# Optimization experiments

Hardware: AMD Instinct MI355X
Metric: run time of the kernel (lower is better)

The kernel has to match this reference:

```python
import jax, jax.numpy as jnp
import numpy as np

N_USERS = 100000
N_LOCAS = 50000
N = N_USERS + N_LOCAS
D = 128   # embedding_dynamic_size
K = 128   # kg entity dim
S = 128   # static dim
NK = 50000  # kg rows
E = 2048  # number of events
LN_EPS = 1e-5
NORM_EPS = 1e-12


def setup_inputs() -> dict:
    key = jax.random.key(0)
    ks = jax.random.split(key, 24)
    f = jnp.float32
    rin = D + K + 1
    s_rnn = 1.0 / np.sqrt(D)
    s_pred = 1.0 / np.sqrt(2 * S + 2 * D + K)
    inp = {
        'embedding': jax.random.normal(ks[0], (N, D), f),
        'static': jax.random.normal(ks[1], (N, S), f),
        'kg': jax.random.normal(ks[2], (NK, K), f),
        'W_ih_u': jax.random.normal(ks[3], (D, rin), f) * s_rnn,
        'b_ih_u': jax.random.normal(ks[4], (D,), f) * s_rnn,
        'W_hh_u': jax.random.normal(ks[5], (D, D), f) * s_rnn,
        'b_hh_u': jax.random.normal(ks[6], (D,), f) * s_rnn,
        'W_ih_l': jax.random.normal(ks[7], (D, rin), f) * s_rnn,
        'b_ih_l': jax.random.normal(ks[8], (D,), f) * s_rnn,
        'W_hh_l': jax.random.normal(ks[9], (D, D), f) * s_rnn,
        'b_hh_l': jax.random.normal(ks[10], (D,), f) * s_rnn,
        'w_proj': jax.random.normal(ks[11], (D,), f),   # NormalLinear(1, D) weight, std=1/sqrt(1)=1
        'b_proj': jax.random.normal(ks[12], (D,), f),
        'ln_g': jnp.ones((D + K,), f),
        'ln_b': jnp.zeros((D + K,), f),
        'W_pred': jax.random.normal(ks[13], (S + D, 2 * S + 2 * D + K), f) * s_pred,
        'b_pred': jnp.zeros((S + D,), f),
        'delta_u': jax.random.uniform(ks[14], (E,), f),
        'delta_l': jax.random.uniform(ks[15], (E,), f),
        'idx_user': jax.random.randint(ks[16], (E,), 0, N_USERS, jnp.int32),
        'idx_loca': jax.random.randint(ks[17], (E,), 0, N_LOCAS, jnp.int32),
        'idx_prev': jax.random.randint(ks[18], (E,), 0, N_LOCAS, jnp.int32),
        'idx_know': jax.random.randint(ks[19], (E,), 0, NK, jnp.int32),
        'num_users': N_USERS,
    }
    return inp


def reference(embedding, static, kg, W_ih_u, b_ih_u, W_hh_u, b_hh_u,
              W_ih_l, b_ih_l, W_hh_l, b_hh_l, w_proj, b_proj, ln_g, ln_b,
              W_pred, b_pred, delta_u, delta_l,
              idx_user, idx_loca, idx_prev, idx_know, num_users):
    sg = jax.lax.stop_gradient

    def l2n(x):  # F.normalize along the feature dim (row vector)
        return x / jnp.maximum(jnp.linalg.norm(x), NORM_EPS)

    # event index preprocessing (matches idx_loca + num_users etc.)
    xs = (idx_user, idx_loca + num_users, idx_prev + num_users, idx_know,
          delta_u, delta_l)

    def step(carry, ev):
        emb, loss = carry
        iu, il, ip, ik, du, dl = ev
        u = emb[iu]        # [D]
        l = emb[il]        # [D]
        p = emb[ip]        # [D]
        kgr = kg[ik]       # [K]
        # projection: u * (1 + Linear(1->D)(delta_u))
        proj = u * (1.0 + w_proj * du + b_proj)
        # layer_norm over concat([emb_prev, kg_row]) of size D+K
        x = jnp.concatenate([p, kgr])
        mu = x.mean()
        var = jnp.mean((x - mu) ** 2)
        ln = (x - mu) / jnp.sqrt(var + LN_EPS) * ln_g + ln_b
        meta = jnp.concatenate([proj, ln, static[ip], static[iu]])  # [2S+2D+K]
        pred = W_pred @ meta + b_pred                               # [S+D]
        tgt = jnp.concatenate([l, static[il]])
        loss_pred = jnp.mean((pred - sg(tgt)) ** 2)
        # RNNCell updates (tanh), then L2-normalize
        x_u = jnp.concatenate([l, kgr, du[None]])
        new_u = l2n(jnp.tanh(W_ih_u @ x_u + b_ih_u + W_hh_u @ u + b_hh_u))
        x_l = jnp.concatenate([u, kgr, dl[None]])
        new_l = l2n(jnp.tanh(W_ih_l @ x_l + b_ih_l + W_hh_l @ l + b_hh_l))
        loss = loss + loss_pred \
                    + jnp.mean((new_u - sg(u)) ** 2) \
                    + jnp.mean((new_l - sg(l)) ** 2)
        emb = emb.at[iu].set(new_u).at[il].set(new_l)
        return (emb, loss), None

    (emb, loss), _ = jax.lax.scan(
        step, (embedding, jnp.asarray(0.0, embedding.dtype)), xs)
    return emb, loss
```

## Files before the change

### kernel.cpp

```cpp
#include <hip/hip_runtime.h>

#define DEVINL static __device__ __forceinline__

typedef float f32x4 __attribute__((ext_vector_type(4)));

constexpr int NUSER = 100000;
constexpr int D     = 128;
constexpr int METAN = 640;
constexpr int NT    = 256;
constexpr int CH    = 4;
constexpr int KP4   = 160;
constexpr int KR4   = 96;
constexpr int NCPY  = 2048;
constexpr int STW   = 640;

struct Params {
  const float *emb_in, *stat, *kg;
  const float *Wihu, *bihu, *Whhu, *bhhu;
  const float *Wihl, *bihl, *Whhl, *bhhl;
  const float *wproj, *bproj, *lng, *lnb, *Wpred, *bpred;
  const float *deltau, *deltal;
  const int *idxu, *idxl, *idxp, *idxk;
  float *emb;
  float *loss_slot;
  float *WpredT;
  float *WrnnT;
  float *brnn;
  float *wcol;
  float *loss_ev;
  float *stash;
  int *cnt_u, *cnt_w, *cnt_t;
  int *flag_u, *flag_l;
  int E, N, NLOC, NWORK;
};

DEVINL float loadx(const float* p) {
  return __hip_atomic_load(p, __ATOMIC_RELAXED, __HIP_MEMORY_SCOPE_AGENT);
}
DEVINL void storex(float* p, float v) {
  __hip_atomic_store(p, v, __ATOMIC_RELAXED, __HIP_MEMORY_SCOPE_AGENT);
}
DEVINL int loadcnt(const int* p) {
  return __hip_atomic_load(p, __ATOMIC_RELAXED, __HIP_MEMORY_SCOPE_AGENT);
}
DEVINL void sigadd(int* pp) {
  __hip_atomic_fetch_add(pp, 1, __ATOMIC_RELAXED, __HIP_MEMORY_SCOPE_AGENT);
}
DEVINL float dot4(float4 a, float4 b) { return a.x*b.x + a.y*b.y + a.z*b.z + a.w*b.w; }

DEVINL float4 block_sum4(float4 v, float4* s4) {
  #pragma unroll
  for (int o = 32; o; o >>= 1) {
    v.x += __shfl_xor(v.x, o, 64); v.y += __shfl_xor(v.y, o, 64);
    v.z += __shfl_xor(v.z, o, 64); v.w += __shfl_xor(v.w, o, 64);
  }
  if ((threadIdx.x & 63) == 0) s4[threadIdx.x >> 6] = v;
  __syncthreads();
  float4 r;
  r.x = s4[0].x + s4[1].x + s4[2].x + s4[3].x;
  r.y = s4[0].y + s4[1].y + s4[2].y + s4[3].y;
  r.z = s4[0].z + s4[1].z + s4[2].z + s4[3].z;
  r.w = s4[0].w + s4[1].w + s4[2].w + s4[3].w;
  __syncthreads();
  return r;
}

DEVINL void half_sum4(float4 v, float4* s4, float4* lo, float4* hi) {
  #pragma unroll
  for (int o = 32; o; o >>= 1) {
    v.x += __shfl_xor(v.x, o, 64); v.y += __shfl_xor(v.y, o, 64);
    v.z += __shfl_xor(v.z, o, 64); v.w += __shfl_xor(v.w, o, 64);
  }
  if ((threadIdx.x & 63) == 0) s4[threadIdx.x >> 6] = v;
  __syncthreads();
  lo->x = s4[0].x + s4[1].x; lo->y = s4[0].y + s4[1].y;
  lo->z = s4[0].z + s4[1].z; lo->w = s4[0].w + s4[1].w;
  hi->x = s4[2].x + s4[3].x; hi->y = s4[2].y + s4[3].y;
  hi->z = s4[2].z + s4[3].z; hi->w = s4[2].w + s4[3].w;
  __syncthreads();
}

__global__ void k_init(Params p) {
  int tid = blockIdx.x * NT + threadIdx.x;
  int stride = gridDim.x * NT;
  for (int e = tid; e < p.E; e += stride) {
    p.flag_u[p.idxu[e]] = 1;
    p.flag_l[p.idxl[e]] = 1;
  }
  for (int idx = tid; idx < 256 * KP4; idx += stride) {
    int j = idx / KP4, k4 = idx - j * KP4;
    float4 v = *(const float4*)(p.Wpred + (size_t)j * METAN + k4 * 4);
    ((float4*)p.WpredT)[k4 * 256 + j] = v;
  }
  for (int idx = tid; idx < 256 * KR4; idx += stride) {
    int j = idx / KR4, k4 = idx - j * KR4;
    int i = j & 127;
    const float* Wih = (j < 128) ? p.Wihu : p.Wihl;
    const float* Whh = (j < 128) ? p.Whhu : p.Whhl;
    float4 v; float* vp = (float*)&v;
    #pragma unroll
    for (int e = 0; e < 4; ++e) {
      int k = k4 * 4 + e;
      vp[e] = (k < 256) ? Wih[(size_t)i * 257 + k] : Whh[(size_t)i * 128 + (k - 256)];
    }
    ((float4*)p.WrnnT)[k4 * 256 + j] = v;
  }
  for (int j = tid; j < 256; j += stride) {
    int i = j & 127;
    p.brnn[j] = (j < 128) ? p.bihu[i] + p.bhhu[i] : p.bihl[i] + p.bhhl[i];
    p.wcol[j] = (j < 128) ? p.Wihu[(size_t)i * 257 + 256] : p.Wihl[(size_t)i * 257 + 256];
  }
}

__global__ __launch_bounds__(NT) void k_copy(Params p) {
  size_t gid = (size_t)blockIdx.x * NT + threadIdx.x;
  size_t gs  = (size_t)gridDim.x * NT;
  size_t n4  = (size_t)p.N * 32;
  const f32x4* src = (const f32x4*)p.emb_in;
  f32x4* dst = (f32x4*)p.emb;
  size_t g = gid;
  for (; g + 3 * gs < n4; g += 4 * gs) {
    size_t g0 = g, g1 = g + gs, g2 = g + 2 * gs, g3 = g + 3 * gs;
    int r0 = (int)(g0 >> 5), r1 = (int)(g1 >> 5), r2 = (int)(g2 >> 5), r3 = (int)(g3 >> 5);
    int f0 = (r0 < NUSER) ? p.flag_u[r0] : p.flag_l[r0 - NUSER];
    int f1 = (r1 < NUSER) ? p.flag_u[r1] : p.flag_l[r1 - NUSER];
    int f2 = (r2 < NUSER) ? p.flag_u[r2] : p.flag_l[r2 - NUSER];
    int f3 = (r3 < NUSER) ? p.flag_u[r3] : p.flag_l[r3 - NUSER];
    f32x4 v0 = src[g0], v1 = src[g1], v2 = src[g2], v3 = src[g3];
    if (!f0) dst[g0] = v0;
    if (!f1) dst[g1] = v1;
    if (!f2) dst[g2] = v2;
    if (!f3) dst[g3] = v3;
  }
  for (; g < n4; g += gs) {
    int r = (int)(g >> 5);
    int f = (r < NUSER) ? p.flag_u[r] : p.flag_l[r - NUSER];
    f32x4 v = src[g];
    if (!f) dst[g] = v;
  }
}

__global__ __launch_bounds__(NT, 2) void k_chain(Params p) {
  __shared__ __align__(16) float s_u[CH][D], s_l[CH][D], s_p[CH][D], s_kg[CH][D];
  __shared__ float4 s_r4[4];
  __shared__ unsigned long long s_redu[4][CH];
  __shared__ int s_ev[8][CH];
  __shared__ float s_dd[2][CH];

  const int tid = threadIdx.x, w = tid >> 6, lane = tid & 63;
  const int c = blockIdx.x;
  const int base = c * CH;
  const int nev = min(CH, p.E - base);
  if (nev <= 0) return;

  int iu_[CH], il_[CH], ip_[CH], ik_[CH];
  float du_[CH], dl_[CH];
  #pragma unroll
  for (int e = 0; e < CH; ++e) {
    int t = base + e; bool v = e < nev;
    iu_[e] = v ? p.idxu[t] : -1;
    il_[e] = v ? p.idxl[t] : -1;
    ip_[e] = v ? p.idxp[t] : -1;
    ik_[e] = v ? p.idxk[t] : 0;
    du_[e] = v ? p.deltau[t] : 0.f;
    dl_[e] = v ? p.deltal[t] : 0.f;
  }

  unsigned long long pk[CH] = {0ull,0ull,0ull,0ull};
  for (int s = tid; s < base; s += NT) {
    int ius = p.idxu[s], ils = p.idxl[s], ips = p.idxp[s];
    #pragma unroll
    for (int e = 0; e < CH; ++e) {
      unsigned long long a  = (ius == iu_[e]);
      unsigned long long wl = (ils == il_[e]);
      unsigned long long b  = (unsigned long long)((ils == il_[e]) + (ips == il_[e]));
      unsigned long long cc = (ils == ip_[e]);
      pk[e] += a | (wl << 16) | (b << 32) | (cc << 48);
    }
  }
  #pragma unroll
  for (int o = 32; o; o >>= 1) {
    #pragma unroll
    for (int e = 0; e < CH; ++e) pk[e] += __shfl_xor(pk[e], o, 64);
  }
  if (lane == 0) {
    #pragma unroll
    for (int e = 0; e < CH; ++e) s_redu[w][e] = pk[e];
  }
  __syncthreads();
  #pragma unroll
  for (int e = 0; e < CH; ++e)
    pk[e] = s_redu[0][e] + s_redu[1][e] + s_redu[2][e] + s_redu[3][e];
  __syncthreads();

  int A_[CH], WL_[CH], B_[CH], C_[CH];
  #pragma unroll
  for (int e = 0; e < CH; ++e) {
    int a  = (int)(pk[e] & 0xffff),        wl = (int)((pk[e] >> 16) & 0xffff);
    int b  = (int)((pk[e] >> 32) & 0xffff), cc = (int)((pk[e] >> 48) & 0xffff);
    #pragma unroll
    for (int s2 = 0; s2 < CH; ++s2) if (s2 < e) {
      a  += (iu_[s2] == iu_[e]);
      wl += (il_[s2] == il_[e]);
      b  += (il_[s2] == il_[e]) + (ip_[s2] == il_[e]);
      cc += (il_[s2] == ip_[e]);
    }
    A_[e] = a; WL_[e] = wl; B_[e] = b; C_[e] = cc;
  }
  bool internal = false;
  #pragma unroll
  for (int t2 = 1; t2 < CH; ++t2) if (t2 < nev) {
    #pragma unroll
    for (int s2 = 0; s2 < t2; ++s2)
      internal |= (iu_[s2] == iu_[t2]) | (il_[s2] == il_[t2]) |
                  (il_[s2] == ip_[t2]) | (ip_[s2] == il_[t2]);
  }

  if (tid == 0) {
    #pragma unroll
    for (int e = 0; e < CH; ++e) {
      s_ev[0][e] = iu_[e]; s_ev[1][e] = il_[e]; s_ev[2][e] = ip_[e];
      s_ev[3][e] = A_[e];  s_ev[4][e] = WL_[e]; s_ev[5][e] = B_[e];
      s_ev[6][e] = C_[e];  s_ev[7][e] = ik_[e];
      s_dd[0][e] = du_[e]; s_dd[1][e] = dl_[e];
    }
  }
  __syncthreads();

  auto PRELOAD = [&](int b0, int b1) {
    int e = w;
    if (e >= b0 && e < b1) {
      int iu = s_ev[0][e], ilr = s_ev[1][e] + NUSER, ipr = s_ev[2][e] + NUSER;
      int A = s_ev[3][e], WL = s_ev[4][e], Ck = s_ev[6][e], ik = s_ev[7][e];
      if (lane < 32) {
        int li = lane * 4;
        *(float4*)&s_kg[e][li] = *(const float4*)(p.kg + (size_t)ik * D + li);
      }
      int i0 = lane * 2;
      if (!A)  *(float2*)&s_u[e][i0] = *(const float2*)(p.emb_in + (size_t)iu  * D + i0);
      if (!WL) *(float2*)&s_l[e][i0] = *(const float2*)(p.emb_in + (size_t)ilr * D + i0);
      if (!Ck) *(float2*)&s_p[e][i0] = *(const float2*)(p.emb_in + (size_t)ipr * D + i0);
    }
  };

  auto SPIN = [&](int b0, int b1) {
    if (w == 0) {
      int e = b0 + lane;
      bool act = lane < (b1 - b0);
      int iu = 0, il = 0, ip = 0, A = 0, Bc = 0, Cc = 0;
      if (act) {
        iu = s_ev[0][e]; il = s_ev[1][e]; ip = s_ev[2][e];
        A = s_ev[3][e]; Bc = s_ev[5][e]; Cc = s_ev[6][e];
      }
      int guard = 0;
      while (true) {
        int x = loadcnt(&p.cnt_u[iu]);
        int y = loadcnt(&p.cnt_t[il]);
        int z = loadcnt(&p.cnt_w[ip]);
        bool ok = (!act) | ((x >= A) & (y >= Bc) & (z >= Cc));
        if (__all(ok)) break;
        if (++guard > (1 << 22)) break;
        __builtin_amdgcn_s_sleep(1);
      }
    }
    __syncthreads();
  };

  auto POSTLOAD = [&](int b0, int b1) {
    int e = w;
    if (e >= b0 && e < b1) {
      int iu = s_ev[0][e], ilr = s_ev[1][e] + NUSER, ipr = s_ev[2][e] + NUSER;
      int A = s_ev[3][e], WL = s_ev[4][e], Ck = s_ev[6][e];
      int i0 = lane * 2;
      if (A) {
        s_u[e][i0]   = loadx(p.emb + (size_t)iu * D + i0);
        s_u[e][i0+1] = loadx(p.emb + (size_t)iu * D + i0 + 1);
      }
      if (WL) {
        s_l[e][i0]   = loadx(p.emb + (size_t)ilr * D + i0);
        s_l[e][i0+1] = loadx(p.emb + (size_t)ilr * D + i0 + 1);
      }
      if (Ck) {
        s_p[e][i0]   = loadx(p.emb + (size_t)ipr * D + i0);
        s_p[e][i0+1] = loadx(p.emb + (size_t)ipr * D + i0 + 1);
      }
    }
  };

  auto RNNPROC = [&](int b0, int b1) {
    __syncthreads();
    const bool uc = (tid < 128);
    const float4* xo0 = (const float4*)(uc ? s_l[0] : s_u[0]);
    const float4* xo1 = (const float4*)(uc ? s_l[1] : s_u[1]);
    const float4* xo2 = (const float4*)(uc ? s_l[2] : s_u[2]);
    const float4* xo3 = (const float4*)(uc ? s_l[3] : s_u[3]);
    const float4* xk0 = (const float4*)s_kg[0];
    const float4* xk1 = (const float4*)s_kg[1];
    const float4* xk2 = (const float4*)s_kg[2];
    const float4* xk3 = (const float4*)s_kg[3];
    const float4* xs0 = (const float4*)(uc ? s_u[0] : s_l[0]);
    const float4* xs1 = (const float4*)(uc ? s_u[1] : s_l[1]);
    const float4* xs2 = (const float4*)(uc ? s_u[2] : s_l[2]);
    const float4* xs3 = (const float4*)(uc ? s_u[3] : s_l[3]);
    float ra0 = 0.f, ra1 = 0.f, ra2 = 0.f, ra3 = 0.f;
    const float4* wr = (const float4*)p.WrnnT + tid;
    #pragma unroll 8
    for (int k4 = 0; k4 < 32; ++k4) {
      float4 wv = wr[k4 * 256];
      ra0 += dot4(wv, xo0[k4]); ra1 += dot4(wv, xo1[k4]);
      ra2 += dot4(wv, xo2[k4]); ra3 += dot4(wv, xo3[k4]);
    }
    #pragma unroll 8
    for (int k4 = 32; k4 < 64; ++k4) {
      float4 wv = wr[k4 * 256];
      ra0 += dot4(wv, xk0[k4-32]); ra1 += dot4(wv, xk1[k4-32]);
      ra2 += dot4(wv, xk2[k4-32]); ra3 += dot4(wv, xk3[k4-32]);
    }
    #pragma unroll 8
    for (int k4 = 64; k4 < 96; ++k4) {
      float4 wv = wr[k4 * 256];
      ra0 += dot4(wv, xs0[k4-64]); ra1 += dot4(wv, xs1[k4-64]);
      ra2 += dot4(wv, xs2[k4-64]); ra3 += dot4(wv, xs3[k4-64]);
    }
    float brn = p.brnn[tid], wcv = p.wcol[tid];
    float d0 = uc ? s_dd[0][0] : s_dd[1][0];
    float d1 = uc ? s_dd[0][1] : s_dd[1][1];
    float d2 = uc ? s_dd[0][2] : s_dd[1][2];
    float d3 = uc ? s_dd[0][3] : s_dd[1][3];
    float h0 = tanhf(ra0 + brn + wcv * d0), h1 = tanhf(ra1 + brn + wcv * d1);
    float h2v = tanhf(ra2 + brn + wcv * d2), h3 = tanhf(ra3 + brn + wcv * d3);

    float4 SU, SL;
    half_sum4(make_float4(h0*h0, h1*h1, h2v*h2v, h3*h3), s_r4, &SU, &SL);
    float s0 = uc ? SU.x : SL.x, s1 = uc ? SU.y : SL.y;
    float s2 = uc ? SU.z : SL.z, s3 = uc ? SU.w : SL.w;
    float n0 = h0 / fmaxf(sqrtf(s0), 1e-12f), n1 = h1 / fmaxf(sqrtf(s1), 1e-12f);
    float n2 = h2v / fmaxf(sqrtf(s2), 1e-12f), n3 = h3 / fmaxf(sqrtf(s3), 1e-12f);

    float nv[CH] = {n0, n1, n2, n3};
    #pragma unroll
    for (int e = 0; e < CH; ++e) if (e >= b0 && e < b1) {
      if (tid < 128) storex(p.emb + (size_t)s_ev[0][e] * D + tid, nv[e]);
      else           storex(p.emb + ((size_t)s_ev[1][e] + NUSER) * D + (tid - 128), nv[e]);
    }
    __syncthreads();

    if (tid >= b0 && tid < b1) {
      __builtin_amdgcn_fence(__ATOMIC_RELEASE, "agent");
      sigadd(&p.cnt_u[s_ev[0][tid]]);
      sigadd(&p.cnt_t[s_ev[1][tid]]);
      sigadd(&p.cnt_w[s_ev[1][tid]]);
      sigadd(&p.cnt_t[s_ev[2][tid]]);
    }

    #pragma unroll
    for (int e = 0; e < CH; ++e) if (e >= b0 && e < b1) {
      float* st = p.stash + (size_t)(base + e) * STW;
      if (tid < 128) {
        st[tid]       = s_u[e][tid];
        st[256 + tid] = s_p[e][tid];
        st[384 + tid] = nv[e];
      } else {
        int i = tid - 128;
        st[128 + i] = s_l[e][i];
        st[512 + i] = nv[e];
      }
    }
  };

  if (!internal) {
    PRELOAD(0, nev);
    SPIN(0, nev);
    POSTLOAD(0, nev);
    RNNPROC(0, nev);
  } else {
    for (int e = 0; e < nev; ++e) {
      PRELOAD(e, e + 1);
      SPIN(e, e + 1);
      POSTLOAD(e, e + 1);
      RNNPROC(e, e + 1);
    }
  }
}

__global__ __launch_bounds__(NT, 2) void k_loss(Params p) {
  __shared__ __align__(16) float s_meta[CH][METAN];
  __shared__ __align__(16) float s_u[CH][D], s_l[CH][D], s_p[CH][D], s_kg[CH][D], s_sil[CH][D];
  __shared__ float4 s_r4[4];

  const int tid = threadIdx.x, w = tid >> 6, lane = tid & 63;
  const int c = blockIdx.x;
  const int base = c * CH;
  const int nev = min(CH, p.E - base);
  if (nev <= 0) return;

  if (w < nev) {
    int e = w;
    int t = base + e;
    int iu = p.idxu[t], ilr = p.idxl[t] + NUSER, ipr = p.idxp[t] + NUSER, ik = p.idxk[t];
    const float* st = p.stash + (size_t)t * STW;
    int i0 = lane * 2;
    *(float2*)&s_u[e][i0] = *(const float2*)(st + i0);
    *(float2*)&s_l[e][i0] = *(const float2*)(st + 128 + i0);
    *(float2*)&s_p[e][i0] = *(const float2*)(st + 256 + i0);
    int h2 = lane >> 5, li = (lane & 31) * 4;
    if (h2 == 0) {
      *(float4*)&s_kg[e][li]         = *(const float4*)(p.kg   + (size_t)ik  * D + li);
      *(float4*)&s_meta[e][512 + li] = *(const float4*)(p.stat + (size_t)iu  * D + li);
    } else {
      *(float4*)&s_meta[e][384 + li] = *(const float4*)(p.stat + (size_t)ipr * D + li);
      *(float4*)&s_sil[e][li]        = *(const float4*)(p.stat + (size_t)ilr * D + li);
    }
  }
  __syncthreads();

  if (w < nev) {
    int e = w;
    float du = p.deltau[base + e];
    float4 xv = (lane < 32) ? *(const float4*)&s_p[e][lane * 4]
                            : *(const float4*)&s_kg[e][(lane - 32) * 4];
    float sm = xv.x + xv.y + xv.z + xv.w;
    #pragma unroll
    for (int o = 32; o; o >>= 1) sm += __shfl_xor(sm, o, 64);
    float mu = sm * (1.f / 256.f);
    float4 d = make_float4(xv.x - mu, xv.y - mu, xv.z - mu, xv.w - mu);
    float vs = d.x*d.x + d.y*d.y + d.z*d.z + d.w*d.w;
    #pragma unroll
    for (int o = 32; o; o >>= 1) vs += __shfl_xor(vs, o, 64);
    float rstd = rsqrtf(vs * (1.f / 256.f) + 1e-5f);
    int idx2 = lane * 4;
    float4 g  = *(const float4*)&p.lng[idx2];
    float4 bb = *(const float4*)&p.lnb[idx2];
    *(float4*)&s_meta[e][128 + idx2] = make_float4(
      d.x*rstd*g.x + bb.x, d.y*rstd*g.y + bb.y,
      d.z*rstd*g.z + bb.z, d.w*rstd*g.w + bb.w);
    int i0 = lane * 2;
    #pragma unroll
    for (int j = 0; j < 2; ++j) {
      int i = i0 + j;
      s_meta[e][i] = s_u[e][i] * (1.f + p.wproj[i] * du + p.bproj[i]);
    }
  }
  __syncthreads();

  const bool uc = (tid < 128);
  const float4* m40 = (const float4*)&s_meta[0][0];
  const float4* m41 = (const float4*)&s_meta[1][0];
  const float4* m42 = (const float4*)&s_meta[2][0];
  const float4* m43 = (const float4*)&s_meta[3][0];
  float pa0 = 0.f, pa1 = 0.f, pa2 = 0.f, pa3 = 0.f;
  const float4* wp = (const float4*)p.WpredT + tid;
  #pragma unroll 8
  for (int k4 = 0; k4 < KP4; ++k4) {
    float4 wv = wp[k4 * 256];
    pa0 += dot4(wv, m40[k4]); pa1 += dot4(wv, m41[k4]);
    pa2 += dot4(wv, m42[k4]); pa3 += dot4(wv, m43[k4]);
  }
  float bp = p.bpred[tid];
  float4 ep2;
  {
    float tg0 = uc ? s_l[0][tid] : s_sil[0][tid - 128];
    float tg1 = uc ? s_l[1][tid] : s_sil[1][tid - 128];
    float tg2 = uc ? s_l[2][tid] : s_sil[2][tid - 128];
    float tg3 = uc ? s_l[3][tid] : s_sil[3][tid - 128];
    float e0 = pa0 + bp - tg0, e1 = pa1 + bp - tg1;
    float e2 = pa2 + bp - tg2, e3 = pa3 + bp - tg3;
    ep2 = make_float4(e0*e0, e1*e1, e2*e2, e3*e3);
  }
  float4 LP = block_sum4(ep2, s_r4);

  const float* st0 = p.stash + (size_t)(base + 0) * STW;
  const float* st1 = p.stash + (size_t)(base + 1) * STW;
  const float* st2 = p.stash + (size_t)(base + 2) * STW;
  const float* st3 = p.stash + (size_t)(base + 3) * STW;
  int noff = uc ? (384 + tid) : (512 + tid - 128);
  float n0 = st0[noff], n1 = (nev > 1) ? st1[noff] : 0.f;
  float n2 = (nev > 2) ? st2[noff] : 0.f, n3 = (nev > 3) ? st3[noff] : 0.f;
  float o0 = uc ? s_u[0][tid] : s_l[0][tid - 128];
  float o1 = uc ? s_u[1][tid] : s_l[1][tid - 128];
  float o2 = uc ? s_u[2][tid] : s_l[2][tid - 128];
  float o3 = uc ? s_u[3][tid] : s_l[3][tid - 128];
  float q0 = n0 - o0, q1 = n1 - o1, q2 = n2 - o2, q3 = n3 - o3;
  float4 LE = block_sum4(make_float4(q0*q0, q1*q1, q2*q2, q3*q3), s_r4);

  if (tid < nev) {
    float lp = (tid == 0) ? LP.x : (tid == 1) ? LP.y : (tid == 2) ? LP.z : LP.w;
    float le = (tid == 0) ? LE.x : (tid == 1) ? LE.y : (tid == 2) ? LE.z : LE.w;
    p.loss_ev[base + tid] = lp * (1.f / 256.f) + le * (1.f / 128.f);
  }
}

__global__ void k_fin(Params p) {
  __shared__ float4 s_r4[4];
  float v = 0.f;
  for (int i = threadIdx.x; i < p.E; i += NT) v += p.loss_ev[i];
  float4 r = block_sum4(make_float4(v, 0.f, 0.f, 0.f), s_r4);
  if (threadIdx.x == 0) p.loss_slot[0] = r.x;
}

extern "C" void kernel_launch(void* const* d_in, const int* in_sizes, int n_in,
                              void* d_out, int out_size, void* d_ws, size_t ws_size,
                              hipStream_t stream) {
  Params p;
  p.emb_in = (const float*)d_in[0];
  p.stat   = (const float*)d_in[1];
  p.kg     = (const float*)d_in[2];
  p.Wihu = (const float*)d_in[3];   p.bihu = (const float*)d_in[4];
  p.Whhu = (const float*)d_in[5];   p.bhhu = (const float*)d_in[6];
  p.Wihl = (const float*)d_in[7];   p.bihl = (const float*)d_in[8];
  p.Whhl = (const float*)d_in[9];   p.bhhl = (const float*)d_in[10];
  p.wproj = (const float*)d_in[11]; p.bproj = (const float*)d_in[12];
  p.lng  = (const float*)d_in[13];  p.lnb  = (const float*)d_in[14];
  p.Wpred = (const float*)d_in[15]; p.bpred = (const float*)d_in[16];
  p.deltau = (const float*)d_in[17];
  p.deltal = (const float*)d_in[18];
  p.idxu = (const int*)d_in[19];
  p.idxl = (const int*)d_in[20];
  p.idxp = (const int*)d_in[21];
  p.idxk = (const int*)d_in[22];

  p.E    = in_sizes[17];
  p.N    = in_sizes[0] / D;
  p.NLOC = p.N - NUSER;
  p.NWORK = (p.E + CH - 1) / CH;

  p.emb       = (float*)d_out;
  p.loss_slot = (float*)d_out + (size_t)p.N * D;

  char* ws = (char*)d_ws;
  size_t off = 0;
  auto take = [&](size_t bytes) {
    void* r = ws + off;
    off += (bytes + 255) & ~(size_t)255;
    return r;
  };
  p.WpredT  = (float*)take((size_t)KP4 * 256 * 16);
  p.WrnnT   = (float*)take((size_t)KR4 * 256 * 16);
  p.brnn    = (float*)take(256 * 4);
  p.wcol    = (float*)take(256 * 4);
  p.loss_ev = (float*)take((size_t)p.E * 4);
  p.stash   = (float*)take((size_t)p.E * STW * 4);
  size_t z0 = off;
  p.cnt_u   = (int*)take((size_t)NUSER * 4);
  p.cnt_w   = (int*)take((size_t)p.NLOC * 4);
  p.cnt_t   = (int*)take((size_t)p.NLOC * 4);
  p.flag_u  = (int*)take((size_t)NUSER * 4);
  p.flag_l  = (int*)take((size_t)p.NLOC * 4);
  size_t zbytes = off - z0;

  hipMemsetAsync(ws + z0, 0, zbytes, stream);
  hipLaunchKernelGGL(k_init,  dim3(512),     dim3(NT), 0, stream, p);
  hipLaunchKernelGGL(k_chain, dim3(p.NWORK), dim3(NT), 0, stream, p);
  hipLaunchKernelGGL(k_copy,  dim3(NCPY),    dim3(NT), 0, stream, p);
  hipLaunchKernelGGL(k_loss,  dim3(p.NWORK), dim3(NT), 0, stream, p);
  hipLaunchKernelGGL(k_fin,   dim3(1),       dim3(NT), 0, stream, p);
}
```

Measured before the change: 178.2 us.

## Fuse chain, loss and copy kernels; precompute dependency info in a prep pass

```diff
diff --git a/kernel.cpp b/kernel.cpp
--- a/kernel.cpp
+++ b/kernel.cpp
@@ -12,7 +12,8 @@
 constexpr int KP4   = 160;
 constexpr int KR4   = 96;
 constexpr int NCPY  = 2048;
-constexpr int STW   = 640;
+constexpr int NINIT = 512;
+constexpr int CIW   = 20;
 
 struct Params {
   const float *emb_in, *stat, *kg;
@@ -28,7 +29,7 @@
   float *brnn;
   float *wcol;
   float *loss_ev;
-  float *stash;
+  int *cinfo;
   int *cnt_u, *cnt_w, *cnt_t;
   int *flag_u, *flag_l;
   int E, N, NLOC, NWORK;
@@ -80,92 +81,56 @@
   __syncthreads();
 }
 
-__global__ void k_init(Params p) {
-  int tid = blockIdx.x * NT + threadIdx.x;
-  int stride = gridDim.x * NT;
-  for (int e = tid; e < p.E; e += stride) {
-    p.flag_u[p.idxu[e]] = 1;
-    p.flag_l[p.idxl[e]] = 1;
-  }
-  for (int idx = tid; idx < 256 * KP4; idx += stride) {
-    int j = idx / KP4, k4 = idx - j * KP4;
-    float4 v = *(const float4*)(p.Wpred + (size_t)j * METAN + k4 * 4);
-    ((float4*)p.WpredT)[k4 * 256 + j] = v;
-  }
-  for (int idx = tid; idx < 256 * KR4; idx += stride) {
-    int j = idx / KR4, k4 = idx - j * KR4;
-    int i = j & 127;
-    const float* Wih = (j < 128) ? p.Wihu : p.Wihl;
-    const float* Whh = (j < 128) ? p.Whhu : p.Whhl;
-    float4 v; float* vp = (float*)&v;
-    #pragma unroll
-    for (int e = 0; e < 4; ++e) {
-      int k = k4 * 4 + e;
-      vp[e] = (k < 256) ? Wih[(size_t)i * 257 + k] : Whh[(size_t)i * 128 + (k - 256)];
-    }
-    ((float4*)p.WrnnT)[k4 * 256 + j] = v;
-  }
-  for (int j = tid; j < 256; j += stride) {
-    int i = j & 127;
-    p.brnn[j] = (j < 128) ? p.bihu[i] + p.bhhu[i] : p.bihl[i] + p.bhhl[i];
-    p.wcol[j] = (j < 128) ? p.Wihu[(size_t)i * 257 + 256] : p.Wihl[(size_t)i * 257 + 256];
-  }
-}
-
-__global__ __launch_bounds__(NT) void k_copy(Params p) {
-  size_t gid = (size_t)blockIdx.x * NT + threadIdx.x;
-  size_t gs  = (size_t)gridDim.x * NT;
-  size_t n4  = (size_t)p.N * 32;
-  const f32x4* src = (const f32x4*)p.emb_in;
-  f32x4* dst = (f32x4*)p.emb;
-  size_t g = gid;
-  for (; g + 3 * gs < n4; g += 4 * gs) {
-    size_t g0 = g, g1 = g + gs, g2 = g + 2 * gs, g3 = g + 3 * gs;
-    int r0 = (int)(g0 >> 5), r1 = (int)(g1 >> 5), r2 = (int)(g2 >> 5), r3 = (int)(g3 >> 5);
-    int f0 = (r0 < NUSER) ? p.flag_u[r0] : p.flag_l[r0 - NUSER];
-    int f1 = (r1 < NUSER) ? p.flag_u[r1] : p.flag_l[r1 - NUSER];
-    int f2 = (r2 < NUSER) ? p.flag_u[r2] : p.flag_l[r2 - NUSER];
-    int f3 = (r3 < NUSER) ? p.flag_u[r3] : p.flag_l[r3 - NUSER];
-    f32x4 v0 = src[g0], v1 = src[g1], v2 = src[g2], v3 = src[g3];
-    if (!f0) dst[g0] = v0;
-    if (!f1) dst[g1] = v1;
-    if (!f2) dst[g2] = v2;
-    if (!f3) dst[g3] = v3;
-  }
-  for (; g < n4; g += gs) {
-    int r = (int)(g >> 5);
-    int f = (r < NUSER) ? p.flag_u[r] : p.flag_l[r - NUSER];
-    f32x4 v = src[g];
-    if (!f) dst[g] = v;
-  }
-}
-
-__global__ __launch_bounds__(NT, 2) void k_chain(Params p) {
-  __shared__ __align__(16) float s_u[CH][D], s_l[CH][D], s_p[CH][D], s_kg[CH][D];
-  __shared__ float4 s_r4[4];
+__global__ __launch_bounds__(NT) void k_prep(Params p) {
+  const int tid = threadIdx.x, w = tid >> 6, lane = tid & 63;
+  const int bid = blockIdx.x;
+
+  if (bid >= p.NWORK) {
+    int gid = (bid - p.NWORK) * NT + tid;
+    int stride = NINIT * NT;
+    for (int e = gid; e < p.E; e += stride) {
+      p.flag_u[p.idxu[e]] = 1;
+      p.flag_l[p.idxl[e]] = 1;
+    }
+    for (int idx = gid; idx < 256 * KP4; idx += stride) {
+      int j = idx / KP4, k4 = idx - j * KP4;
+      float4 v = *(const float4*)(p.Wpred + (size_t)j * METAN + k4 * 4);
+      ((float4*)p.WpredT)[k4 * 256 + j] = v;
+    }
+    for (int idx = gid; idx < 256 * KR4; idx += stride) {
+      int j = idx / KR4, k4 = idx - j * KR4;
+      int i = j & 127;
+      const float* Wih = (j < 128) ? p.Wihu : p.Wihl;
+      const float* Whh = (j < 128) ? p.Whhu : p.Whhl;
+      float4 v; float* vp = (float*)&v;
+      #pragma unroll
+      for (int e = 0; e < 4; ++e) {
+        int k = k4 * 4 + e;
+        vp[e] = (k < 256) ? Wih[(size_t)i * 257 + k] : Whh[(size_t)i * 128 + (k - 256)];
+      }
+      ((float4*)p.WrnnT)[k4 * 256 + j] = v;
+    }
+    for (int j = gid; j < 256; j += stride) {
+      int i = j & 127;
+      p.brnn[j] = (j < 128) ? p.bihu[i] + p.bhhu[i] : p.bihl[i] + p.bhhl[i];
+      p.wcol[j] = (j < 128) ? p.Wihu[(size_t)i * 257 + 256] : p.Wihl[(size_t)i * 257 + 256];
+    }
+    return;
+  }
+
   __shared__ unsigned long long s_redu[4][CH];
-  __shared__ int s_ev[8][CH];
-  __shared__ float s_dd[2][CH];
-
-  const int tid = threadIdx.x, w = tid >> 6, lane = tid & 63;
-  const int c = blockIdx.x;
-  const int base = c * CH;
+  const int c = bid, base = c * CH;
   const int nev = min(CH, p.E - base);
   if (nev <= 0) return;
 
-  int iu_[CH], il_[CH], ip_[CH], ik_[CH];
-  float du_[CH], dl_[CH];
+  int iu_[CH], il_[CH], ip_[CH];
   #pragma unroll
   for (int e = 0; e < CH; ++e) {
     int t = base + e; bool v = e < nev;
     iu_[e] = v ? p.idxu[t] : -1;
     il_[e] = v ? p.idxl[t] : -1;
     ip_[e] = v ? p.idxp[t] : -1;
-    ik_[e] = v ? p.idxk[t] : 0;
-    du_[e] = v ? p.deltau[t] : 0.f;
-    dl_[e] = v ? p.deltal[t] : 0.f;
-  }
-
+  }
   unsigned long long pk[CH] = {0ull,0ull,0ull,0ull};
   for (int s = tid; s < base; s += NT) {
     int ius = p.idxu[s], ils = p.idxl[s], ips = p.idxp[s];
@@ -191,57 +156,118 @@
   #pragma unroll
   for (int e = 0; e < CH; ++e)
     pk[e] = s_redu[0][e] + s_redu[1][e] + s_redu[2][e] + s_redu[3][e];
-  __syncthreads();
-
-  int A_[CH], WL_[CH], B_[CH], C_[CH];
-  #pragma unroll
-  for (int e = 0; e < CH; ++e) {
-    int a  = (int)(pk[e] & 0xffff),        wl = (int)((pk[e] >> 16) & 0xffff);
-    int b  = (int)((pk[e] >> 32) & 0xffff), cc = (int)((pk[e] >> 48) & 0xffff);
-    #pragma unroll
-    for (int s2 = 0; s2 < CH; ++s2) if (s2 < e) {
-      a  += (iu_[s2] == iu_[e]);
-      wl += (il_[s2] == il_[e]);
-      b  += (il_[s2] == il_[e]) + (ip_[s2] == il_[e]);
-      cc += (il_[s2] == ip_[e]);
-    }
-    A_[e] = a; WL_[e] = wl; B_[e] = b; C_[e] = cc;
-  }
-  bool internal = false;
-  #pragma unroll
-  for (int t2 = 1; t2 < CH; ++t2) if (t2 < nev) {
-    #pragma unroll
-    for (int s2 = 0; s2 < t2; ++s2)
-      internal |= (iu_[s2] == iu_[t2]) | (il_[s2] == il_[t2]) |
-                  (il_[s2] == ip_[t2]) | (ip_[s2] == il_[t2]);
-  }
 
   if (tid == 0) {
+    int* ci = p.cinfo + (size_t)c * CIW;
+    bool internal = false;
+    #pragma unroll
+    for (int t2 = 1; t2 < CH; ++t2) if (t2 < nev) {
+      #pragma unroll
+      for (int s2 = 0; s2 < t2; ++s2)
+        internal |= (iu_[s2] == iu_[t2]) | (il_[s2] == il_[t2]) |
+                    (il_[s2] == ip_[t2]) | (ip_[s2] == il_[t2]);
+    }
+    bool clean = !internal;
     #pragma unroll
     for (int e = 0; e < CH; ++e) {
-      s_ev[0][e] = iu_[e]; s_ev[1][e] = il_[e]; s_ev[2][e] = ip_[e];
-      s_ev[3][e] = A_[e];  s_ev[4][e] = WL_[e]; s_ev[5][e] = B_[e];
-      s_ev[6][e] = C_[e];  s_ev[7][e] = ik_[e];
-      s_dd[0][e] = du_[e]; s_dd[1][e] = dl_[e];
-    }
-  }
-  __syncthreads();
-
-  auto PRELOAD = [&](int b0, int b1) {
+      int a  = (int)(pk[e] & 0xffff),        wl = (int)((pk[e] >> 16) & 0xffff);
+      int b  = (int)((pk[e] >> 32) & 0xffff), cc = (int)((pk[e] >> 48) & 0xffff);
+      #pragma unroll
+      for (int s2 = 0; s2 < CH; ++s2) if (s2 < e) {
+        a  += (iu_[s2] == iu_[e]);
+        wl += (il_[s2] == il_[e]);
+        b  += (il_[s2] == il_[e]) + (ip_[s2] == il_[e]);
+        cc += (il_[s2] == ip_[e]);
+      }
+      ci[e] = a; ci[4 + e] = wl; ci[8 + e] = b; ci[12 + e] = cc;
+      if (e < nev) clean = clean && (a == 0) && (b == 0) && (cc == 0);
+    }
+    ci[16] = internal ? 1 : 0;
+    ci[17] = clean ? 1 : 0;
+  }
+}
+
+__global__ __launch_bounds__(NT, 2) void k_main(Params p) {
+  const int tid = threadIdx.x, w = tid >> 6, lane = tid & 63;
+  const int bid = blockIdx.x;
+
+  if (bid >= p.NWORK) {
+    size_t gid = (size_t)(bid - p.NWORK) * NT + tid;
+    size_t gs  = (size_t)NCPY * NT;
+    size_t n4  = (size_t)p.N * 32;
+    const f32x4* src = (const f32x4*)p.emb_in;
+    f32x4* dst = (f32x4*)p.emb;
+    size_t g = gid;
+    for (; g + 3 * gs < n4; g += 4 * gs) {
+      size_t g0 = g, g1 = g + gs, g2 = g + 2 * gs, g3 = g + 3 * gs;
+      int r0 = (int)(g0 >> 5), r1 = (int)(g1 >> 5), r2 = (int)(g2 >> 5), r3 = (int)(g3 >> 5);
+      int f0 = (r0 < NUSER) ? p.flag_u[r0] : p.flag_l[r0 - NUSER];
+      int f1 = (r1 < NUSER) ? p.flag_u[r1] : p.flag_l[r1 - NUSER];
+      int f2 = (r2 < NUSER) ? p.flag_u[r2] : p.flag_l[r2 - NUSER];
+      int f3 = (r3 < NUSER) ? p.flag_u[r3] : p.flag_l[r3 - NUSER];
+      f32x4 v0 = src[g0], v1 = src[g1], v2 = src[g2], v3 = src[g3];
+      if (!f0) dst[g0] = v0;
+      if (!f1) dst[g1] = v1;
+      if (!f2) dst[g2] = v2;
+      if (!f3) dst[g3] = v3;
+    }
+    for (; g < n4; g += gs) {
+      int r = (int)(g >> 5);
+      int f = (r < NUSER) ? p.flag_u[r] : p.flag_l[r - NUSER];
+      f32x4 v = src[g];
+      if (!f) dst[g] = v;
+    }
+    return;
+  }
+
+  __shared__ __align__(16) float s_meta[CH][METAN];
+  __shared__ __align__(16) float s_u[CH][D], s_l[CH][D], s_p[CH][D], s_kg[CH][D], s_sil[CH][D];
+  __shared__ float4 s_r4[4];
+  __shared__ int s_ev[8][CH];
+  __shared__ float s_dd[2][CH];
+
+  const int c = bid, base = c * CH;
+  const int nev = min(CH, p.E - base);
+  if (nev <= 0) return;
+  const int* ci = p.cinfo + (size_t)c * CIW;
+  const int internal = ci[16];
+  const int clean    = ci[17];
+
+  if (tid == 0) {
+    #pragma unroll
+    for (int e = 0; e < CH; ++e) {
+      int t = base + e; bool v = e < nev;
+      s_ev[0][e] = v ? p.idxu[t] : 0;
+      s_ev[1][e] = v ? p.idxl[t] : 0;
+      s_ev[2][e] = v ? p.idxp[t] : 0;
+      s_ev[3][e] = ci[e];
+      s_ev[4][e] = ci[4 + e];
+      s_ev[5][e] = ci[8 + e];
+      s_ev[6][e] = ci[12 + e];
+      s_ev[7][e] = v ? p.idxk[t] : 0;
+      s_dd[0][e] = v ? p.deltau[t] : 0.f;
+      s_dd[1][e] = v ? p.deltal[t] : 0.f;
+    }
+  }
+  __syncthreads();
+
+  if (w < nev) {
     int e = w;
-    if (e >= b0 && e < b1) {
-      int iu = s_ev[0][e], ilr = s_ev[1][e] + NUSER, ipr = s_ev[2][e] + NUSER;
-      int A = s_ev[3][e], WL = s_ev[4][e], Ck = s_ev[6][e], ik = s_ev[7][e];
-      if (lane < 32) {
-        int li = lane * 4;
-        *(float4*)&s_kg[e][li] = *(const float4*)(p.kg + (size_t)ik * D + li);
-      }
-      int i0 = lane * 2;
-      if (!A)  *(float2*)&s_u[e][i0] = *(const float2*)(p.emb_in + (size_t)iu  * D + i0);
-      if (!WL) *(float2*)&s_l[e][i0] = *(const float2*)(p.emb_in + (size_t)ilr * D + i0);
-      if (!Ck) *(float2*)&s_p[e][i0] = *(const float2*)(p.emb_in + (size_t)ipr * D + i0);
-    }
-  };
+    int iu = s_ev[0][e], ilr = s_ev[1][e] + NUSER, ipr = s_ev[2][e] + NUSER;
+    int A = s_ev[3][e], WL = s_ev[4][e], Ck = s_ev[6][e], ik = s_ev[7][e];
+    int h2 = lane >> 5, li = (lane & 31) * 4;
+    if (h2 == 0) {
+      *(float4*)&s_kg[e][li]         = *(const float4*)(p.kg   + (size_t)ik  * D + li);
+      *(float4*)&s_meta[e][512 + li] = *(const float4*)(p.stat + (size_t)iu  * D + li);
+    } else {
+      *(float4*)&s_meta[e][384 + li] = *(const float4*)(p.stat + (size_t)ipr * D + li);
+      *(float4*)&s_sil[e][li]        = *(const float4*)(p.stat + (size_t)ilr * D + li);
+    }
+    int i0 = lane * 2;
+    if (!A)  *(float2*)&s_u[e][i0] = *(const float2*)(p.emb_in + (size_t)iu  * D + i0);
+    if (!WL) *(float2*)&s_l[e][i0] = *(const float2*)(p.emb_in + (size_t)ilr * D + i0);
+    if (!Ck) *(float2*)&s_p[e][i0] = *(const float2*)(p.emb_in + (size_t)ipr * D + i0);
+  }
 
   auto SPIN = [&](int b0, int b1) {
     if (w == 0) {
@@ -287,9 +313,11 @@
     }
   };
 
+  float nvkeep[CH] = {0.f, 0.f, 0.f, 0.f};
+  const bool uc = (tid < 128);
+
   auto RNNPROC = [&](int b0, int b1) {
     __syncthreads();
-    const bool uc = (tid < 128);
     const float4* xo0 = (const float4*)(uc ? s_l[0] : s_u[0]);
     const float4* xo1 = (const float4*)(uc ? s_l[1] : s_u[1]);
     const float4* xo2 = (const float4*)(uc ? s_l[2] : s_u[2]);
@@ -337,6 +365,11 @@
     float n0 = h0 / fmaxf(sqrtf(s0), 1e-12f), n1 = h1 / fmaxf(sqrtf(s1), 1e-12f);
     float n2 = h2v / fmaxf(sqrtf(s2), 1e-12f), n3 = h3 / fmaxf(sqrtf(s3), 1e-12f);
 
+    if (b0 <= 0 && 0 < b1) nvkeep[0] = n0;
+    if (b0 <= 1 && 1 < b1) nvkeep[1] = n1;
+    if (b0 <= 2 && 2 < b1) nvkeep[2] = n2;
+    if (b0 <= 3 && 3 < b1) nvkeep[3] = n3;
+
     float nv[CH] = {n0, n1, n2, n3};
     #pragma unroll
     for (int e = 0; e < CH; ++e) if (e >= b0 && e < b1) {
@@ -352,71 +385,28 @@
       sigadd(&p.cnt_w[s_ev[1][tid]]);
       sigadd(&p.cnt_t[s_ev[2][tid]]);
     }
-
-    #pragma unroll
-    for (int e = 0; e < CH; ++e) if (e >= b0 && e < b1) {
-      float* st = p.stash + (size_t)(base + e) * STW;
-      if (tid < 128) {
-        st[tid]       = s_u[e][tid];
-        st[256 + tid] = s_p[e][tid];
-        st[384 + tid] = nv[e];
-      } else {
-        int i = tid - 128;
-        st[128 + i] = s_l[e][i];
-        st[512 + i] = nv[e];
-      }
-    }
   };
 
-  if (!internal) {
-    PRELOAD(0, nev);
+  if (clean) {
+    RNNPROC(0, nev);
+  } else if (!internal) {
     SPIN(0, nev);
     POSTLOAD(0, nev);
     RNNPROC(0, nev);
   } else {
-    for (int e = 0; e < nev; ++e) {
-      PRELOAD(e, e + 1);
-      SPIN(e, e + 1);
-      POSTLOAD(e, e + 1);
-      RNNPROC(e, e + 1);
-    }
-  }
-}
-
-__global__ __launch_bounds__(NT, 2) void k_loss(Params p) {
-  __shared__ __align__(16) float s_meta[CH][METAN];
-  __shared__ __align__(16) float s_u[CH][D], s_l[CH][D], s_p[CH][D], s_kg[CH][D], s_sil[CH][D];
-  __shared__ float4 s_r4[4];
-
-  const int tid = threadIdx.x, w = tid >> 6, lane = tid & 63;
-  const int c = blockIdx.x;
-  const int base = c * CH;
-  const int nev = min(CH, p.E - base);
-  if (nev <= 0) return;
+    #pragma unroll
+    for (int e = 0; e < CH; ++e) {
+      if (e < nev) {
+        SPIN(e, e + 1);
+        POSTLOAD(e, e + 1);
+        RNNPROC(e, e + 1);
+      }
+    }
+  }
 
   if (w < nev) {
     int e = w;
-    int t = base + e;
-    int iu = p.idxu[t], ilr = p.idxl[t] + NUSER, ipr = p.idxp[t] + NUSER, ik = p.idxk[t];
-    const float* st = p.stash + (size_t)t * STW;
-    int i0 = lane * 2;
-    *(float2*)&s_u[e][i0] = *(const float2*)(st + i0);
-    *(float2*)&s_l[e][i0] = *(const float2*)(st + 128 + i0);
-    *(float2*)&s_p[e][i0] = *(const float2*)(st + 256 + i0);
-    int h2 = lane >> 5, li = (lane & 31) * 4;
-    if (h2 == 0) {
-      *(float4*)&s_kg[e][li]         = *(const float4*)(p.kg   + (size_t)ik  * D + li);
-      *(float4*)&s_meta[e][512 + li] = *(const float4*)(p.stat + (size_t)iu  * D + li);
-    } else {
-      *(float4*)&s_meta[e][384 + li] = *(const float4*)(p.stat + (size_t)ipr * D + li);
-      *(float4*)&s_sil[e][li]        = *(const float4*)(p.stat + (size_t)ilr * D + li);
-    }
-  }
-  __syncthreads();
-
-  if (w < nev) {
-    int e = w;
-    float du = p.deltau[base + e];
+    float du = s_dd[0][e];
     float4 xv = (lane < 32) ? *(const float4*)&s_p[e][lane * 4]
                             : *(const float4*)&s_kg[e][(lane - 32) * 4];
     float sm = xv.x + xv.y + xv.z + xv.w;
@@ -443,7 +433,6 @@
   }
   __syncthreads();
 
-  const bool uc = (tid < 128);
   const float4* m40 = (const float4*)&s_meta[0][0];
   const float4* m41 = (const float4*)&s_meta[1][0];
   const float4* m42 = (const float4*)&s_meta[2][0];
@@ -469,18 +458,12 @@
   }
   float4 LP = block_sum4(ep2, s_r4);
 
-  const float* st0 = p.stash + (size_t)(base + 0) * STW;
-  const float* st1 = p.stash + (size_t)(base + 1) * STW;
-  const float* st2 = p.stash + (size_t)(base + 2) * STW;
-  const float* st3 = p.stash + (size_t)(base + 3) * STW;
-  int noff = uc ? (384 + tid) : (512 + tid - 128);
-  float n0 = st0[noff], n1 = (nev > 1) ? st1[noff] : 0.f;
-  float n2 = (nev > 2) ? st2[noff] : 0.f, n3 = (nev > 3) ? st3[noff] : 0.f;
   float o0 = uc ? s_u[0][tid] : s_l[0][tid - 128];
   float o1 = uc ? s_u[1][tid] : s_l[1][tid - 128];
   float o2 = uc ? s_u[2][tid] : s_l[2][tid - 128];
   float o3 = uc ? s_u[3][tid] : s_l[3][tid - 128];
-  float q0 = n0 - o0, q1 = n1 - o1, q2 = n2 - o2, q3 = n3 - o3;
+  float q0 = nvkeep[0] - o0, q1 = nvkeep[1] - o1;
+  float q2 = nvkeep[2] - o2, q3 = nvkeep[3] - o3;
   float4 LE = block_sum4(make_float4(q0*q0, q1*q1, q2*q2, q3*q3), s_r4);
 
   if (tid < nev) {
@@ -539,7 +522,7 @@
   p.brnn    = (float*)take(256 * 4);
   p.wcol    = (float*)take(256 * 4);
   p.loss_ev = (float*)take((size_t)p.E * 4);
-  p.stash   = (float*)take((size_t)p.E * STW * 4);
+  p.cinfo   = (int*)take((size_t)p.NWORK * CIW * 4);
   size_t z0 = off;
   p.cnt_u   = (int*)take((size_t)NUSER * 4);
   p.cnt_w   = (int*)take((size_t)p.NLOC * 4);
@@ -549,9 +532,7 @@
   size_t zbytes = off - z0;
 
   hipMemsetAsync(ws + z0, 0, zbytes, stream);
-  hipLaunchKernelGGL(k_init,  dim3(512),     dim3(NT), 0, stream, p);
-  hipLaunchKernelGGL(k_chain, dim3(p.NWORK), dim3(NT), 0, stream, p);
-  hipLaunchKernelGGL(k_copy,  dim3(NCPY),    dim3(NT), 0, stream, p);
-  hipLaunchKernelGGL(k_loss,  dim3(p.NWORK), dim3(NT), 0, stream, p);
-  hipLaunchKernelGGL(k_fin,   dim3(1),       dim3(NT), 0, stream, p);
-}
+  hipLaunchKernelGGL(k_prep, dim3(p.NWORK + NINIT), dim3(NT), 0, stream, p);
+  hipLaunchKernelGGL(k_main, dim3(p.NWORK + NCPY),  dim3(NT), 0, stream, p);
+  hipLaunchKernelGGL(k_fin,  dim3(1),               dim3(NT), 0, stream, p);
+}
```

Result: faster. 151.5 us (-15.0%).
